# Performance work log

Measured on AMD Instinct MI355X. Metric: run time of the kernel, lower is better.

Reference implementation:

```python
import jax, jax.numpy as jnp
import numpy as np
import math

N = 400000  # total anchors across FPN levels
M = 128     # GT boxes per image
IOU_LOW, IOU_HIGH = 0.3, 0.6
SCALE_CLAMP = math.log(224.0 / 8.0)
NEUTRAL = -1.0e8


def setup_inputs() -> dict:
    key = jax.random.key(0)
    k1, k2, k3, k4, k5, k6 = jax.random.split(key, 6)
    # anchors: valid XYXY boxes centered in an 800x800 image
    ctr = jax.random.uniform(k1, (N, 2), minval=0.0, maxval=800.0)
    half = jax.random.uniform(k2, (N, 2), minval=8.0, maxval=64.0)
    anchors = jnp.concatenate([ctr - half, ctr + half], axis=1)
    deltas = jax.random.normal(k3, (N, 4)) * 0.2
    # GT boxes (M, 5): XYXY + class id
    gctr = jax.random.uniform(k4, (M, 2), minval=0.0, maxval=800.0)
    ghalf = jax.random.uniform(k5, (M, 2), minval=10.0, maxval=120.0)
    cls = jnp.floor(jax.random.uniform(k6, (M, 1), minval=0.0, maxval=20.0))
    gt_boxes = jnp.concatenate([gctr - ghalf, gctr + ghalf, cls], axis=1)
    return {"anchors": anchors, "deltas": deltas, "gt_boxes": gt_boxes}


def apply_deltas_to_anchors(deltas, anchors):
    # mirrors rcnn_apply_deltas_to_anchors (note: pw/ph are HALF widths/heights)
    dx = deltas[:, 0]
    dy = deltas[:, 1]
    dw = jnp.minimum(deltas[:, 2], SCALE_CLAMP)
    dh = jnp.minimum(deltas[:, 3], SCALE_CLAMP)
    px = (anchors[:, 0] + anchors[:, 2]) * 0.5
    py = (anchors[:, 1] + anchors[:, 3]) * 0.5
    pw = (anchors[:, 2] - anchors[:, 0]) * 0.5
    ph = (anchors[:, 3] - anchors[:, 1]) * 0.5
    bx = px + pw * dx
    by = py + ph * dy
    bw = pw * jnp.exp(dw)
    bh = ph * jnp.exp(dh)
    return jnp.stack([bx - bw, by - bh, bx + bw, by + bh], axis=-1)


def pairwise_iou(b1, b2):
    # (Nm, 4) x (Nn, 4) -> (Nm, Nn), XYXY format, mirrors iou()
    x1 = jnp.maximum(b1[:, None, 0], b2[None, :, 0])
    y1 = jnp.maximum(b1[:, None, 1], b2[None, :, 1])
    x2 = jnp.minimum(b1[:, None, 2], b2[None, :, 2])
    y2 = jnp.minimum(b1[:, None, 3], b2[None, :, 3])
    xl = x2 - x1
    yl = y2 - y1
    inter = jnp.where((xl > 0) & (yl > 0), xl * yl, 0.0)
    area1 = (b1[:, 2] - b1[:, 0]) * (b1[:, 3] - b1[:, 1])
    area2 = (b2[:, 2] - b2[:, 0]) * (b2[:, 3] - b2[:, 1])
    union = area1[:, None] + area2[None, :] - inter
    return inter / union


def reference(anchors, deltas, gt_boxes):
    proposals = apply_deltas_to_anchors(deltas, anchors)
    # 2) match anchors to GT (rcnn_match_anchors_to_gt).
    #    Invalid GT (class == -1) are masked out of the IoU matrix instead of
    #    filtered (keeps static shapes under jit).
    valid = gt_boxes[:, 4] != -1
    m = pairwise_iou(anchors, gt_boxes[:, :4])          # (N, M)
    m = jnp.where(valid[None, :], m, -1.0)
    match_quality = jnp.max(m, axis=1)                   # (N,)
    matched_idxs = jnp.argmax(m, axis=1)                 # (N,)
    matched_gt = gt_boxes[matched_idxs]                  # (N, 5)
    matched_gt = jnp.where((match_quality <= IOU_LOW)[:, None], -1.0, matched_gt)
    neutral = (match_quality > IOU_LOW) & (match_quality < IOU_HIGH)
    matched_gt = jnp.where(neutral[:, None], NEUTRAL, matched_gt)
    return proposals, matched_gt
```

## Files before the change

kernel.cpp:

```cpp
#include <hip/hip_runtime.h>
#include <math.h>

typedef float v2f __attribute__((ext_vector_type(2)));

__device__ __forceinline__ v2f v2_min(v2f a, float b) {
    v2f r; r.x = fminf(a.x, b); r.y = fminf(a.y, b); return r;
}
__device__ __forceinline__ v2f v2_max(v2f a, float b) {
    v2f r; r.x = fmaxf(a.x, b); r.y = fmaxf(a.y, b); return r;
}
__device__ __forceinline__ v2f v2_max0(v2f a) {
    v2f r; r.x = fmaxf(a.x, 0.0f); r.y = fmaxf(a.y, 0.0f); return r;
}

__global__ void prep_kernel(const float* __restrict__ gt, float* __restrict__ pre, int m) {
    int j = threadIdx.x;
    if (j < m) {
        float g0 = gt[j * 5 + 0];
        float g1 = gt[j * 5 + 1];
        float g2 = gt[j * 5 + 2];
        float g3 = gt[j * 5 + 3];
        float g4 = gt[j * 5 + 4];
        bool valid = (g4 != -1.0f);
        float* p = pre + j * 8;
        if (valid) {
            p[0] = g0; p[1] = g1; p[2] = g2; p[3] = g3;
            p[4] = (g2 - g0) * (g3 - g1);
        } else {
            p[0] = 1e30f; p[1] = 1e30f; p[2] = -1e30f; p[3] = -1e30f;
            p[4] = 0.0f;
        }
        p[5] = g4; p[6] = 0.0f; p[7] = 0.0f;
    }
}

__global__ __launch_bounds__(256) void rpn_match_kernel(
    const float* __restrict__ anchors,
    const float* __restrict__ deltas,
    const float* __restrict__ pre,
    float* __restrict__ out,
    int n, int m)
{
    const int tid = threadIdx.x;
    const int i0 = blockIdx.x * 512 + tid;
    const int i1 = i0 + 256;
    const bool v0 = (i0 < n);
    const bool v1 = (i1 < n);
    const int i0c = v0 ? i0 : 0;
    const int i1c = v1 ? i1 : 0;

    const float4 a0 = reinterpret_cast<const float4*>(anchors)[i0c];
    const float4 a1 = reinterpret_cast<const float4*>(anchors)[i1c];
    const float4 d0 = reinterpret_cast<const float4*>(deltas)[i0c];
    const float4 d1 = reinterpret_cast<const float4*>(deltas)[i1c];

    const float SCALE_CLAMP = 3.3322045101752038f;
    {
        float pw = (a0.z - a0.x) * 0.5f, ph = (a0.w - a0.y) * 0.5f;
        float px = (a0.x + a0.z) * 0.5f, py = (a0.y + a0.w) * 0.5f;
        float bx = px + pw * d0.x, by = py + ph * d0.y;
        float bw = pw * expf(fminf(d0.z, SCALE_CLAMP));
        float bh = ph * expf(fminf(d0.w, SCALE_CLAMP));
        if (v0) reinterpret_cast<float4*>(out)[i0] =
            make_float4(bx - bw, by - bh, bx + bw, by + bh);
    }
    {
        float pw = (a1.z - a1.x) * 0.5f, ph = (a1.w - a1.y) * 0.5f;
        float px = (a1.x + a1.z) * 0.5f, py = (a1.y + a1.w) * 0.5f;
        float bx = px + pw * d1.x, by = py + ph * d1.y;
        float bw = pw * expf(fminf(d1.z, SCALE_CLAMP));
        float bh = ph * expf(fminf(d1.w, SCALE_CLAMP));
        if (v1) reinterpret_cast<float4*>(out)[i1] =
            make_float4(bx - bw, by - bh, bx + bw, by + bh);
    }

    v2f ax; ax.x = a0.x; ax.y = a1.x;
    v2f ay; ay.x = a0.y; ay.y = a1.y;
    v2f az; az.x = a0.z; az.y = a1.z;
    v2f aw; aw.x = a0.w; aw.y = a1.w;
    v2f ar; ar.x = (a0.z - a0.x) * (a0.w - a0.y);
            ar.y = (a1.z - a1.x) * (a1.w - a1.y);

    const float4* p4 = reinterpret_cast<const float4*>(pre);

    v2f bI, bS;
    int bidx0 = 0, bidx1 = 0;
    {
        float4 b = p4[0];
        float ga = p4[1].x;
        v2f xl = v2_min(az, b.z) - v2_max(ax, b.x);
        v2f yl = v2_min(aw, b.w) - v2_max(ay, b.y);
        bI = v2_max0(xl) * v2_max0(yl);
        bS = ar + ga;
    }

    #pragma unroll 8
    for (int j = 1; j < m; ++j) {
        float4 b  = p4[2 * j];
        float  ga = p4[2 * j + 1].x;
        v2f xl = v2_min(az, b.z) - v2_max(ax, b.x);
        v2f yl = v2_min(aw, b.w) - v2_max(ay, b.y);
        v2f inter = v2_max0(xl) * v2_max0(yl);
        v2f S = ar + ga;
        v2f lhs = inter * bS;
        v2f rhs = bI * S;
        bool g0 = lhs.x > rhs.x;
        bool g1 = lhs.y > rhs.y;
        bI.x  = g0 ? inter.x : bI.x;
        bS.x  = g0 ? S.x     : bS.x;
        bidx0 = g0 ? j       : bidx0;
        bI.y  = g1 ? inter.y : bI.y;
        bS.y  = g1 ? S.y     : bS.y;
        bidx1 = g1 ? j       : bidx1;
    }

    const float IOU_LOW = 0.3f, IOU_HIGH = 0.6f, NEUTRAL = -100000000.0f;
    float* mout = out + (size_t)n * 4;

    {
        float uni = bS.x - bI.x;
        float q = bI.x / uni;
        float o0, o1, o2, o3, o4;
        if (q <= IOU_LOW) {
            o0 = o1 = o2 = o3 = o4 = -1.0f;
        } else if (q < IOU_HIGH) {
            o0 = o1 = o2 = o3 = o4 = NEUTRAL;
        } else {
            float4 gbx = p4[2 * bidx0];
            o0 = gbx.x; o1 = gbx.y; o2 = gbx.z; o3 = gbx.w;
            o4 = p4[2 * bidx0 + 1].y;
        }
        if (v0) {
            float* mo = mout + (size_t)i0 * 5;
            mo[0] = o0; mo[1] = o1; mo[2] = o2; mo[3] = o3; mo[4] = o4;
        }
    }
    {
        float uni = bS.y - bI.y;
        float q = bI.y / uni;
        float o0, o1, o2, o3, o4;
        if (q <= IOU_LOW) {
            o0 = o1 = o2 = o3 = o4 = -1.0f;
        } else if (q < IOU_HIGH) {
            o0 = o1 = o2 = o3 = o4 = NEUTRAL;
        } else {
            float4 gbx = p4[2 * bidx1];
            o0 = gbx.x; o1 = gbx.y; o2 = gbx.z; o3 = gbx.w;
            o4 = p4[2 * bidx1 + 1].y;
        }
        if (v1) {
            float* mo = mout + (size_t)i1 * 5;
            mo[0] = o0; mo[1] = o1; mo[2] = o2; mo[3] = o3; mo[4] = o4;
        }
    }
}

extern "C" void kernel_launch(void* const* d_in, const int* in_sizes, int n_in,
                              void* d_out, int out_size, void* d_ws, size_t ws_size,
                              hipStream_t stream) {
    const float* anchors  = (const float*)d_in[0];
    const float* deltas   = (const float*)d_in[1];
    const float* gt_boxes = (const float*)d_in[2];
    float* out = (float*)d_out;
    float* pre = (float*)d_ws;

    int n = in_sizes[0] / 4;
    int m = in_sizes[2] / 5;

    hipLaunchKernelGGL(prep_kernel, dim3(1), dim3(256), 0, stream, gt_boxes, pre, m);

    int nblocks = (n + 511) / 512;
    hipLaunchKernelGGL(rpn_match_kernel, dim3(nblocks), dim3(256), 0, stream,
                       anchors, deltas, pre, out, n, m);
}
```

Baseline: 99.55 us.

## Fuse GT preprocessing into match kernel and stage GT boxes in LDS

```diff
diff --git a/kernel.cpp b/kernel.cpp
--- a/kernel.cpp
+++ b/kernel.cpp
@@ -1,5 +1,7 @@
 #include <hip/hip_runtime.h>
 #include <math.h>
+
+#define MAX_GT 128
 
 typedef float v2f __attribute__((ext_vector_type(2)));
 
@@ -13,35 +15,30 @@
     v2f r; r.x = fmaxf(a.x, 0.0f); r.y = fmaxf(a.y, 0.0f); return r;
 }
 
-__global__ void prep_kernel(const float* __restrict__ gt, float* __restrict__ pre, int m) {
-    int j = threadIdx.x;
-    if (j < m) {
-        float g0 = gt[j * 5 + 0];
-        float g1 = gt[j * 5 + 1];
-        float g2 = gt[j * 5 + 2];
-        float g3 = gt[j * 5 + 3];
-        float g4 = gt[j * 5 + 4];
-        bool valid = (g4 != -1.0f);
-        float* p = pre + j * 8;
-        if (valid) {
-            p[0] = g0; p[1] = g1; p[2] = g2; p[3] = g3;
-            p[4] = (g2 - g0) * (g3 - g1);
-        } else {
-            p[0] = 1e30f; p[1] = 1e30f; p[2] = -1e30f; p[3] = -1e30f;
-            p[4] = 0.0f;
-        }
-        p[5] = g4; p[6] = 0.0f; p[7] = 0.0f;
-    }
-}
-
 __global__ __launch_bounds__(256) void rpn_match_kernel(
     const float* __restrict__ anchors,
     const float* __restrict__ deltas,
-    const float* __restrict__ pre,
+    const float* __restrict__ gt_boxes,
     float* __restrict__ out,
     int n, int m)
 {
+    __shared__ float4 sbox[MAX_GT];
+    __shared__ float  scls[MAX_GT];
+
     const int tid = threadIdx.x;
+    if (tid < m) {
+        float g0 = gt_boxes[tid * 5 + 0];
+        float g1 = gt_boxes[tid * 5 + 1];
+        float g2 = gt_boxes[tid * 5 + 2];
+        float g3 = gt_boxes[tid * 5 + 3];
+        float g4 = gt_boxes[tid * 5 + 4];
+        bool valid = (g4 != -1.0f);
+        sbox[tid] = valid ? make_float4(g0, g1, g2, g3)
+                          : make_float4(0.0f, 0.0f, 0.0f, 0.0f);
+        scls[tid] = g4;
+    }
+    __syncthreads();
+
     const int i0 = blockIdx.x * 512 + tid;
     const int i1 = i0 + 256;
     const bool v0 = (i0 < n);
@@ -81,23 +78,14 @@
     v2f ar; ar.x = (a0.z - a0.x) * (a0.w - a0.y);
             ar.y = (a1.z - a1.x) * (a1.w - a1.y);
 
-    const float4* p4 = reinterpret_cast<const float4*>(pre);
-
-    v2f bI, bS;
+    v2f bI; bI.x = -1.0f; bI.y = -1.0f;
+    v2f bS; bS.x =  1.0f; bS.y =  1.0f;
     int bidx0 = 0, bidx1 = 0;
-    {
-        float4 b = p4[0];
-        float ga = p4[1].x;
-        v2f xl = v2_min(az, b.z) - v2_max(ax, b.x);
-        v2f yl = v2_min(aw, b.w) - v2_max(ay, b.y);
-        bI = v2_max0(xl) * v2_max0(yl);
-        bS = ar + ga;
-    }
 
     #pragma unroll 8
-    for (int j = 1; j < m; ++j) {
-        float4 b  = p4[2 * j];
-        float  ga = p4[2 * j + 1].x;
+    for (int j = 0; j < m; ++j) {
+        float4 b = sbox[j];
+        float ga = (b.z - b.x) * (b.w - b.y);
         v2f xl = v2_min(az, b.z) - v2_max(ax, b.x);
         v2f yl = v2_min(aw, b.w) - v2_max(ay, b.y);
         v2f inter = v2_max0(xl) * v2_max0(yl);
@@ -126,9 +114,8 @@
         } else if (q < IOU_HIGH) {
             o0 = o1 = o2 = o3 = o4 = NEUTRAL;
         } else {
-            float4 gbx = p4[2 * bidx0];
-            o0 = gbx.x; o1 = gbx.y; o2 = gbx.z; o3 = gbx.w;
-            o4 = p4[2 * bidx0 + 1].y;
+            float4 gbx = sbox[bidx0];
+            o0 = gbx.x; o1 = gbx.y; o2 = gbx.z; o3 = gbx.w; o4 = scls[bidx0];
         }
         if (v0) {
             float* mo = mout + (size_t)i0 * 5;
@@ -144,9 +131,8 @@
         } else if (q < IOU_HIGH) {
             o0 = o1 = o2 = o3 = o4 = NEUTRAL;
         } else {
-            float4 gbx = p4[2 * bidx1];
-            o0 = gbx.x; o1 = gbx.y; o2 = gbx.z; o3 = gbx.w;
-            o4 = p4[2 * bidx1 + 1].y;
+            float4 gbx = sbox[bidx1];
+            o0 = gbx.x; o1 = gbx.y; o2 = gbx.z; o3 = gbx.w; o4 = scls[bidx1];
         }
         if (v1) {
             float* mo = mout + (size_t)i1 * 5;
@@ -162,14 +148,11 @@
     const float* deltas   = (const float*)d_in[1];
     const float* gt_boxes = (const float*)d_in[2];
     float* out = (float*)d_out;
-    float* pre = (float*)d_ws;
 
     int n = in_sizes[0] / 4;
     int m = in_sizes[2] / 5;
 
-    hipLaunchKernelGGL(prep_kernel, dim3(1), dim3(256), 0, stream, gt_boxes, pre, m);
-
     int nblocks = (n + 511) / 512;
     hipLaunchKernelGGL(rpn_match_kernel, dim3(nblocks), dim3(256), 0, stream,
-                       anchors, deltas, pre, out, n, m);
+                       anchors, deltas, gt_boxes, out, n, m);
 }
```

Measured after the change: 98.59 us. Within noise of the previous version (-1.0%).
